# Kernel tuning notes

Measured on AMD Instinct MI355X. Metric: run time of the kernel, lower is better.

The kernel has to match this reference:

```python
import jax, jax.numpy as jnp
import numpy as np

D = 1024
ITERATIONS = 2


def setup_inputs() -> dict:
    key = jax.random.key(0)
    ks = jax.random.split(key, 7)
    s = 1.0 / np.sqrt(D)  # PyTorch GRUCell/Linear init scale
    x = jax.random.normal(ks[0], (8, 4096, D), dtype=jnp.float32)
    W_ih = jax.random.uniform(ks[1], (3 * D, D), minval=-s, maxval=s, dtype=jnp.float32)
    W_hh = jax.random.uniform(ks[2], (3 * D, D), minval=-s, maxval=s, dtype=jnp.float32)
    b_ih = jax.random.uniform(ks[3], (3 * D,), minval=-s, maxval=s, dtype=jnp.float32)
    b_hh = jax.random.uniform(ks[4], (3 * D,), minval=-s, maxval=s, dtype=jnp.float32)
    We = jax.random.uniform(ks[5], (1, D), minval=-s, maxval=s, dtype=jnp.float32)
    be = jax.random.uniform(ks[6], (1,), minval=-s, maxval=s, dtype=jnp.float32)
    return {"x": x, "W_ih": W_ih, "W_hh": W_hh, "b_ih": b_ih, "b_hh": b_hh, "We": We, "be": be}


def _gru_cell(inp, h, W_ih, W_hh, b_ih, b_hh):
    # PyTorch GRUCell gate order: r, z, n
    gi = inp @ W_ih.T + b_ih  # [N, 3D]
    gh = h @ W_hh.T + b_hh    # [N, 3D]
    i_r, i_z, i_n = jnp.split(gi, 3, axis=-1)
    h_r, h_z, h_n = jnp.split(gh, 3, axis=-1)
    r = jax.nn.sigmoid(i_r + h_r)
    z = jax.nn.sigmoid(i_z + h_z)
    n = jnp.tanh(i_n + r * h_n)
    return (1.0 - z) * n + z * h


def reference(x, W_ih, W_hh, b_ih, b_hh, We, be):
    B, S, Dm = x.shape
    state = x.reshape(-1, Dm)  # [B*S, D]
    for _ in range(ITERATIONS):
        error = jax.nn.sigmoid(state @ We.T + be)  # [B*S, 1]
        new_state = _gru_cell(state, state, W_ih, W_hh, b_ih, b_hh)
        state = (1.0 - error) * state + error * new_state
    return state.reshape(B, S, Dm)
```

## Files before the change

### kernel.cpp

```cpp
#include <hip/hip_runtime.h>

#define DD 1024

typedef int   i32x4  __attribute__((ext_vector_type(4)));
typedef int   i32x8  __attribute__((ext_vector_type(8)));
typedef float f32x16 __attribute__((ext_vector_type(16)));

__device__ __forceinline__ float sigm(float x) { return 1.0f / (1.0f + __expf(-x)); }
__device__ __forceinline__ float tanh_fast(float x) {
  float e = __expf(-2.0f * fabsf(x));
  float t = (1.0f - e) / (1.0f + e);
  return copysignf(t, x);
}
__device__ __forceinline__ void gload_lds16(const void* g, void* l) {
  __builtin_amdgcn_global_load_lds((const __attribute__((address_space(1))) void*)g,
                                   (__attribute__((address_space(3))) void*)l, 16, 0, 0);
}
__device__ __forceinline__ unsigned pk_fp8x4(float a, float b, float c, float d) {
  int u = __builtin_amdgcn_cvt_pk_fp8_f32(a, b, 0, false);
  u = __builtin_amdgcn_cvt_pk_fp8_f32(c, d, u, true);
  return (unsigned)u;
}


__global__ __launch_bounds__(256) void prep_weights(
    const float* __restrict__ Wih, const float* __restrict__ Whh,
    const float* __restrict__ bih, const float* __restrict__ bhh,
    unsigned char* __restrict__ Wcat8, float* __restrict__ bias) {
  int i = blockIdx.x * 256 + threadIdx.x;
  int g = i >> 18;
  int rem = i & 262143;
  int n = rem >> 8;
  int k4 = rem & 255;
  const float4* wih4 = reinterpret_cast<const float4*>(Wih);
  const float4* whh4 = reinterpret_cast<const float4*>(Whh);
  float4 v;
  if (g == 0) {
    size_t idx = (size_t)n * 256 + k4;
    float4 a = wih4[idx], b = whh4[idx];
    v = make_float4(a.x + b.x, a.y + b.y, a.z + b.z, a.w + b.w);
  } else if (g == 1) {
    size_t idx = (size_t)(DD + n) * 256 + k4;
    float4 a = wih4[idx], b = whh4[idx];
    v = make_float4(a.x + b.x, a.y + b.y, a.z + b.z, a.w + b.w);
  } else if (g == 2) {
    size_t idx = (size_t)(2 * DD + n) * 256 + k4;
    v = wih4[idx];
  } else {
    size_t idx = (size_t)(2 * DD + n) * 256 + k4;
    v = whh4[idx];
  }
  unsigned pkd = pk_fp8x4(v.x * 32.0f, v.y * 32.0f, v.z * 32.0f, v.w * 32.0f);

  int db   = n >> 5;
  int dgl  = n & 31;
  int kt   = k4 >> 4;
  int gran = (k4 >> 2) & 3;
  int sel  = ((gran & 1) << 1) | (gran >> 1);
  int klo  = (k4 & 3) * 4;
  size_t addr = (size_t)db * 131072 + (size_t)kt * 8192 + g * 2048 +
                sel * 512 + dgl * 16 + klo;
  *reinterpret_cast<unsigned*>(Wcat8 + addr) = pkd;

  if (i < 4 * DD) {
    int bg = i >> 10, bn = i & 1023;
    float bv;
    if (bg == 0)      bv = bih[bn] + bhh[bn];
    else if (bg == 1) bv = bih[DD + bn] + bhh[DD + bn];
    else if (bg == 2) bv = bih[2 * DD + bn];
    else              bv = bhh[2 * DD + bn];
    bias[i] = bv;
  }
}

__global__ __launch_bounds__(256) void error_cast(
    const float* S, const float* __restrict__ We, const float* __restrict__ be,
    unsigned char* __restrict__ Sb8, float* __restrict__ err) {
  __shared__ float part[4];
  const int row = blockIdx.x;
  const int t = threadIdx.x;
  float4 v = reinterpret_cast<const float4*>(S + (size_t)row * DD)[t];
  float4 w = reinterpret_cast<const float4*>(We)[t];
  float dot = v.x * w.x + v.y * w.y + v.z * w.z + v.w * w.w;

  int r    = row & 127;
  int kt   = t >> 4;
  int gran = (t >> 2) & 3;
  int sel  = ((gran & 1) << 1) | (gran >> 1);
  int klo  = (t & 3) * 4;
  size_t addr = (size_t)(row >> 7) * 131072 + (size_t)kt * 8192 +
                (r >> 5) * 2048 + sel * 512 + (r & 31) * 16 + klo;
  *reinterpret_cast<unsigned*>(Sb8 + addr) = pk_fp8x4(v.x, v.y, v.z, v.w);

#pragma unroll
  for (int off = 32; off > 0; off >>= 1) dot += __shfl_xor(dot, off);
  if ((t & 63) == 0) part[t >> 6] = dot;
  __syncthreads();
  if (t == 0) err[row] = sigm(part[0] + part[1] + part[2] + part[3] + be[0]);
}

__global__ __launch_bounds__(256, 4) void gru_fused_gemm(
    const unsigned char* __restrict__ Sb8,
    const unsigned char* __restrict__ Wcat8,
    const float* __restrict__ bias,
    const float* __restrict__ err,
    const float* Sf,
    float* out, int M) {
  __shared__ alignas(16) unsigned char As[2 * 8192];
  __shared__ alignas(16) unsigned char Bs[2 * 8192];

  const int bid = blockIdx.x;
  const int x = bid & 7;
  const int c = bid >> 3;
  const int db = (x & 1) * 16 + (c & 15);
  const int rb = (x >> 1) * 64 + (c >> 4);

  const int tid = threadIdx.x;
  const int w = tid >> 6;
  const int lane = tid & 63;
  const int l31 = lane & 31;
  const int h = lane >> 5;

  const unsigned char* sA0 = Sb8 + (size_t)rb * 131072 + (size_t)w * 1024 + lane * 16;
  const unsigned char* sB0 = Wcat8 + (size_t)db * 131072 + (size_t)w * 1024 + lane * 16;
  unsigned char* const dA0 = As + w * 1024;
  unsigned char* const dB0 = Bs + w * 1024;

  const int aoff = w * 2048 + h * 512 + l31 * 16;
  const int bq = h * 512 + l31 * 16;

  f32x16 acc[4];
#pragma unroll
  for (int g = 0; g < 4; ++g)
#pragma unroll
    for (int r = 0; r < 16; ++r) acc[g][r] = 0.0f;

  auto stage = [&](int t) {
    const int slot = (t & 1) * 8192;
    const size_t koff = (size_t)t * 8192;
    gload_lds16(sA0 + koff, dA0 + slot);
    gload_lds16(sA0 + koff + 4096, dA0 + slot + 4096);
    gload_lds16(sB0 + koff, dB0 + slot);
    gload_lds16(sB0 + koff + 4096, dB0 + slot + 4096);
  };

  stage(0);
  stage(1);

#pragma unroll
  for (int t = 0; t < 16; ++t) {
    const int sb = (t & 1) * 8192;
    if (t < 15) asm volatile("s_waitcnt vmcnt(4)" ::: "memory");
    else        asm volatile("s_waitcnt vmcnt(0)" ::: "memory");
    __builtin_amdgcn_s_barrier();

    const unsigned char* Ab = As + sb;
    const unsigned char* Bb = Bs + sb;
    i32x4 a0 = *reinterpret_cast<const i32x4*>(Ab + aoff);
    i32x4 a1 = *reinterpret_cast<const i32x4*>(Ab + aoff + 1024);
    i32x8 a = __builtin_shufflevector(a0, a1, 0, 1, 2, 3, 4, 5, 6, 7);
    i32x8 bf[4];
#pragma unroll
    for (int g = 0; g < 4; ++g) {
      i32x4 b0 = *reinterpret_cast<const i32x4*>(Bb + g * 2048 + bq);
      i32x4 b1 = *reinterpret_cast<const i32x4*>(Bb + g * 2048 + bq + 1024);
      bf[g] = __builtin_shufflevector(b0, b1, 0, 1, 2, 3, 4, 5, 6, 7);
    }
    asm volatile("s_waitcnt lgkmcnt(0)" ::: "memory");
    __builtin_amdgcn_s_barrier();

    if (t <= 13) stage(t + 2);

    __builtin_amdgcn_s_setprio(1);
#pragma unroll
    for (int g = 0; g < 4; ++g)
      acc[g] = __builtin_amdgcn_mfma_scale_f32_32x32x64_f8f6f4(
          a, bf[g], acc[g], 0, 0, 0, 127, 0, 122);
    __builtin_amdgcn_s_setprio(0);
  }

  const int dgcol = db * 32 + l31;
  const float b_r = bias[dgcol];
  const float b_z = bias[DD + dgcol];
  const float b_i = bias[2 * DD + dgcol];
  const float b_h = bias[3 * DD + dgcol];
#pragma unroll
  for (int reg = 0; reg < 16; ++reg) {
    int rowf = (reg & 3) + 8 * (reg >> 2) + 4 * h;
    int m = rb * 128 + w * 32 + rowf;
    float e = err[m];
    float hh = Sf[(size_t)m * DD + dgcol];
    float r = sigm(acc[0][reg] + b_r);
    float z = sigm(acc[1][reg] + b_z);
    float n = tanh_fast(acc[2][reg] + b_i + r * (acc[3][reg] + b_h));
    out[(size_t)m * DD + dgcol] = hh + e * (1.0f - z) * (n - hh);
  }
}

extern "C" void kernel_launch(void* const* d_in, const int* in_sizes, int n_in,
                              void* d_out, int out_size, void* d_ws, size_t ws_size,
                              hipStream_t stream) {
  const float* x   = (const float*)d_in[0];
  const float* Wih = (const float*)d_in[1];
  const float* Whh = (const float*)d_in[2];
  const float* bih = (const float*)d_in[3];
  const float* bhh = (const float*)d_in[4];
  const float* We  = (const float*)d_in[5];
  const float* be  = (const float*)d_in[6];
  float* out = (float*)d_out;
  const int M = in_sizes[0] / DD;

  char* ws = (char*)d_ws;
  unsigned char* Sb8   = (unsigned char*)ws;
  unsigned char* Wcat8 = (unsigned char*)(ws + (size_t)M * DD);
  float* bias = (float*)(ws + (size_t)M * DD + (size_t)4 * DD * DD);
  float* err  = (float*)(ws + (size_t)M * DD + (size_t)4 * DD * DD + (size_t)4 * DD * 4);

  prep_weights<<<4096, 256, 0, stream>>>(Wih, Whh, bih, bhh, Wcat8, bias);

  const int nwg = (M / 128) * 32;
  const float* S = x;
  for (int it = 0; it < 2; ++it) {
    error_cast<<<M, 256, 0, stream>>>(S, We, be, Sb8, err);
    gru_fused_gemm<<<nwg, 256, 0, stream>>>(Sb8, Wcat8, bias, err, S, out, M);
    S = out;
  }
}
```

Before: 439.9 us.

## Double M tile to 256 rows and load A fragments directly from global

Each workgroup now computes 256 rows instead of 128, with every wave holding two 32-row A fragments, so each weight tile staged in LDS feeds twice as many MFMAs. The A operand no longer goes through LDS. It is loaded straight from global memory into registers, double-buffered one k-step ahead. Accumulator registers double, so occupancy drops to two blocks per CU, and direct global A loads may expose more latency.

```diff
diff --git a/kernel.cpp b/kernel.cpp
--- a/kernel.cpp
+++ b/kernel.cpp
@@ -99,21 +99,20 @@
   if (t == 0) err[row] = sigm(part[0] + part[1] + part[2] + part[3] + be[0]);
 }
 
-__global__ __launch_bounds__(256, 4) void gru_fused_gemm(
+__global__ __launch_bounds__(256, 2) void gru_fused_gemm(
     const unsigned char* __restrict__ Sb8,
     const unsigned char* __restrict__ Wcat8,
     const float* __restrict__ bias,
     const float* __restrict__ err,
     const float* Sf,
     float* out, int M) {
-  __shared__ alignas(16) unsigned char As[2 * 8192];
   __shared__ alignas(16) unsigned char Bs[2 * 8192];
 
   const int bid = blockIdx.x;
   const int x = bid & 7;
   const int c = bid >> 3;
   const int db = (x & 1) * 16 + (c & 15);
-  const int rb = (x >> 1) * 64 + (c >> 4);
+  const int mb = (x >> 1) * 32 + (c >> 4);
 
   const int tid = threadIdx.x;
   const int w = tid >> 6;
@@ -121,63 +120,94 @@
   const int l31 = lane & 31;
   const int h = lane >> 5;
 
-  const unsigned char* sA0 = Sb8 + (size_t)rb * 131072 + (size_t)w * 1024 + lane * 16;
   const unsigned char* sB0 = Wcat8 + (size_t)db * 131072 + (size_t)w * 1024 + lane * 16;
-  unsigned char* const dA0 = As + w * 1024;
   unsigned char* const dB0 = Bs + w * 1024;
 
-  const int aoff = w * 2048 + h * 512 + l31 * 16;
+  const unsigned char* aptr[2];
+#pragma unroll
+  for (int f = 0; f < 2; ++f) {
+    int rg = 2 * w + f;
+    aptr[f] = Sb8 + (size_t)(2 * mb + (rg >> 2)) * 131072 +
+              (rg & 3) * 2048 + h * 512 + l31 * 16;
+  }
   const int bq = h * 512 + l31 * 16;
 
-  f32x16 acc[4];
-#pragma unroll
-  for (int g = 0; g < 4; ++g)
-#pragma unroll
-    for (int r = 0; r < 16; ++r) acc[g][r] = 0.0f;
-
-  auto stage = [&](int t) {
+  f32x16 acc[2][4];
+#pragma unroll
+  for (int f = 0; f < 2; ++f)
+#pragma unroll
+    for (int g = 0; g < 4; ++g)
+#pragma unroll
+      for (int r = 0; r < 16; ++r) acc[f][g][r] = 0.0f;
+
+  i32x8 aX[2], aY[2];
+
+#define LOAD_A(T, DST)                                                         \
+  {                                                                            \
+    _Pragma("unroll")                                                          \
+    for (int f = 0; f < 2; ++f) {                                              \
+      const unsigned char* p = aptr[f] + (size_t)(T) * 8192;                   \
+      i32x4 lo = *reinterpret_cast<const i32x4*>(p);                           \
+      i32x4 hi = *reinterpret_cast<const i32x4*>(p + 1024);                    \
+      DST[f] = __builtin_shufflevector(lo, hi, 0, 1, 2, 3, 4, 5, 6, 7);        \
+    }                                                                          \
+  }
+
+  auto stageB = [&](int t) {
     const int slot = (t & 1) * 8192;
     const size_t koff = (size_t)t * 8192;
-    gload_lds16(sA0 + koff, dA0 + slot);
-    gload_lds16(sA0 + koff + 4096, dA0 + slot + 4096);
     gload_lds16(sB0 + koff, dB0 + slot);
     gload_lds16(sB0 + koff + 4096, dB0 + slot + 4096);
   };
 
-  stage(0);
-  stage(1);
+  LOAD_A(0, aX)
+  stageB(0);
+  stageB(1);
 
 #pragma unroll
   for (int t = 0; t < 16; ++t) {
-    const int sb = (t & 1) * 8192;
-    if (t < 15) asm volatile("s_waitcnt vmcnt(4)" ::: "memory");
+    if (t < 15) asm volatile("s_waitcnt vmcnt(2)" ::: "memory");
     else        asm volatile("s_waitcnt vmcnt(0)" ::: "memory");
     __builtin_amdgcn_s_barrier();
 
-    const unsigned char* Ab = As + sb;
-    const unsigned char* Bb = Bs + sb;
-    i32x4 a0 = *reinterpret_cast<const i32x4*>(Ab + aoff);
-    i32x4 a1 = *reinterpret_cast<const i32x4*>(Ab + aoff + 1024);
-    i32x8 a = __builtin_shufflevector(a0, a1, 0, 1, 2, 3, 4, 5, 6, 7);
+    if (t <= 14) {
+      if ((t & 1) == 0) LOAD_A(t + 1, aY)
+      else              LOAD_A(t + 1, aX)
+    }
+
+    const int sb = (t & 1) * 8192;
     i32x8 bf[4];
 #pragma unroll
     for (int g = 0; g < 4; ++g) {
-      i32x4 b0 = *reinterpret_cast<const i32x4*>(Bb + g * 2048 + bq);
-      i32x4 b1 = *reinterpret_cast<const i32x4*>(Bb + g * 2048 + bq + 1024);
+      i32x4 b0 = *reinterpret_cast<const i32x4*>(Bs + sb + g * 2048 + bq);
+      i32x4 b1 = *reinterpret_cast<const i32x4*>(Bs + sb + g * 2048 + bq + 1024);
       bf[g] = __builtin_shufflevector(b0, b1, 0, 1, 2, 3, 4, 5, 6, 7);
     }
     asm volatile("s_waitcnt lgkmcnt(0)" ::: "memory");
     __builtin_amdgcn_s_barrier();
 
-    if (t <= 13) stage(t + 2);
-
+    if (t <= 13) stageB(t + 2);
+
+    asm volatile("" ::: "memory");
     __builtin_amdgcn_s_setprio(1);
-#pragma unroll
-    for (int g = 0; g < 4; ++g)
-      acc[g] = __builtin_amdgcn_mfma_scale_f32_32x32x64_f8f6f4(
-          a, bf[g], acc[g], 0, 0, 0, 127, 0, 122);
+    if ((t & 1) == 0) {
+#pragma unroll
+      for (int g = 0; g < 4; ++g)
+#pragma unroll
+        for (int f = 0; f < 2; ++f)
+          acc[f][g] = __builtin_amdgcn_mfma_scale_f32_32x32x64_f8f6f4(
+              aX[f], bf[g], acc[f][g], 0, 0, 0, 127, 0, 122);
+    } else {
+#pragma unroll
+      for (int g = 0; g < 4; ++g)
+#pragma unroll
+        for (int f = 0; f < 2; ++f)
+          acc[f][g] = __builtin_amdgcn_mfma_scale_f32_32x32x64_f8f6f4(
+              aY[f], bf[g], acc[f][g], 0, 0, 0, 127, 0, 122);
+    }
     __builtin_amdgcn_s_setprio(0);
   }
+#undef LOAD_A
 
   const int dgcol = db * 32 + l31;
   const float b_r = bias[dgcol];
@@ -185,15 +215,18 @@
   const float b_i = bias[2 * DD + dgcol];
   const float b_h = bias[3 * DD + dgcol];
 #pragma unroll
-  for (int reg = 0; reg < 16; ++reg) {
-    int rowf = (reg & 3) + 8 * (reg >> 2) + 4 * h;
-    int m = rb * 128 + w * 32 + rowf;
-    float e = err[m];
-    float hh = Sf[(size_t)m * DD + dgcol];
-    float r = sigm(acc[0][reg] + b_r);
-    float z = sigm(acc[1][reg] + b_z);
-    float n = tanh_fast(acc[2][reg] + b_i + r * (acc[3][reg] + b_h));
-    out[(size_t)m * DD + dgcol] = hh + e * (1.0f - z) * (n - hh);
+  for (int f = 0; f < 2; ++f) {
+#pragma unroll
+    for (int reg = 0; reg < 16; ++reg) {
+      int rowf = (reg & 3) + 8 * (reg >> 2) + 4 * h;
+      int m = mb * 256 + w * 64 + f * 32 + rowf;
+      float e = err[m];
+      float hh = Sf[(size_t)m * DD + dgcol];
+      float r = sigm(acc[f][0][reg] + b_r);
+      float z = sigm(acc[f][1][reg] + b_z);
+      float n = tanh_fast(acc[f][2][reg] + b_i + r * (acc[f][3][reg] + b_h));
+      out[(size_t)m * DD + dgcol] = hh + e * (1.0f - z) * (n - hh);
+    }
   }
 }
 
@@ -218,7 +251,7 @@
 
   prep_weights<<<4096, 256, 0, stream>>>(Wih, Whh, bih, bhh, Wcat8, bias);
 
-  const int nwg = (M / 128) * 32;
+  const int nwg = (M / 256) * 32;
   const float* S = x;
   for (int it = 0; it < 2; ++it) {
     error_cast<<<M, 256, 0, stream>>>(S, We, be, Sb8, err);
```

Result: slower. 479.9 us (+9.1%).
